# Optimization experiments

Hardware: AMD Instinct MI355X
Metric: run time of the kernel (lower is better)

Reference implementation:

```python
import jax, jax.numpy as jnp
import numpy as np
import math

B, S = 4, 1024
N_ITEMS, EMB = 50000, 128
H, D = 4, 32


def setup_inputs() -> dict:
    key = jax.random.key(0)
    ks = jax.random.split(key, 12)

    def lin(k, fan_in, fan_out):
        lim = 1.0 / math.sqrt(fan_in)
        return jax.random.uniform(k, (fan_in, fan_out), minval=-lim, maxval=lim, dtype=jnp.float32)

    inp = {}
    inp["sequence_item_indices"] = jax.random.randint(ks[0], (B, S), 0, N_ITEMS, dtype=jnp.int32)
    inp["sequence_correct_flags"] = jax.random.randint(ks[1], (B, S), 0, 2, dtype=jnp.int32)
    inp["sequence_time_gaps"] = jax.random.uniform(ks[2], (B, S), dtype=jnp.float32) * 100.0
    inp["item_emb"] = jax.random.normal(ks[3], (N_ITEMS, EMB), dtype=jnp.float32) * 0.02
    inp["ans_emb"] = jax.random.normal(ks[4], (2, EMB), dtype=jnp.float32) * 0.02
    inp["Wq"] = lin(ks[5], EMB, H * D); inp["bq"] = jnp.zeros((H * D,), jnp.float32)
    inp["Wk"] = lin(ks[6], EMB, H * D); inp["bk"] = jnp.zeros((H * D,), jnp.float32)
    inp["Wv"] = lin(ks[7], EMB, H * D); inp["bv"] = jnp.zeros((H * D,), jnp.float32)
    inp["Wh"] = lin(ks[8], 2 * EMB, EMB); inp["bh"] = jnp.zeros((EMB,), jnp.float32)
    inp["W1"] = lin(ks[9], H * D + EMB, EMB); inp["b1"] = jnp.zeros((EMB,), jnp.float32)
    inp["W2"] = lin(ks[10], EMB, 1); inp["b2"] = jnp.zeros((1,), jnp.float32)
    inp["theta_raw"] = jnp.zeros((H,), jnp.float32)
    return inp


def reference(sequence_item_indices, sequence_correct_flags, sequence_time_gaps,
              item_emb, ans_emb, Wq, bq, Wk, bk, Wv, bv, Wh, bh, W1, b1, W2, b2, theta_raw):
    Bb, Ss = sequence_item_indices.shape
    Hn = theta_raw.shape[0]
    Dd = Wq.shape[1] // Hn

    e = item_emb[sequence_item_indices]                      # [B,S,E]
    a = ans_emb[sequence_correct_flags]                      # [B,S,E]
    inter = jnp.concatenate([e, a], axis=-1) @ Wh + bh       # history_projection

    Q = (e @ Wq + bq).reshape(Bb, Ss, Hn, Dd)
    K = (e @ Wk + bk).reshape(Bb, Ss, Hn, Dd)
    V = (inter @ Wv + bv).reshape(Bb, Ss, Hn, Dd)
    scale = 1.0 / jnp.sqrt(jnp.float32(Dd))

    # self relevance per history position; per-target softmax over i<t done via exclusive prefix sums
    sr = jnp.sum(Q * K, axis=-1) * scale                     # [B,S,H]
    ex = jnp.exp(sr - jnp.max(sr, axis=1, keepdims=True))    # shift-invariant
    Ep = jnp.concatenate([jnp.zeros((Bb, 1, Hn), sr.dtype), jnp.cumsum(ex, axis=1)], axis=1)  # [B,S+1,H]

    g = jnp.maximum(sequence_time_gaps.astype(jnp.float32), 1.0)
    Pp = jnp.concatenate([jnp.zeros((Bb, 1), g.dtype), jnp.cumsum(g, axis=1)], axis=1)        # [B,S+1]

    t = jnp.arange(1, Ss)                                    # targets, T = S-1
    i = jnp.arange(Ss)                                       # history positions
    mask = i[None, :] < t[:, None]                           # [T,S]
    step = (t[:, None] - i[None, :]).astype(jnp.float32)     # arange(L,0,-1)[i] == t - i
    gap_diff = Pp[:, 1:Ss, None] - Pp[:, None, :Ss]          # [B,T,S]  sum_{j in [i,t)} clamp(gap,1)
    Et = Ep[:, 1:Ss, :]                                      # [B,T,H]  softmax normalizer Z_t
    rel = (Et[:, :, None, :] - Ep[:, None, :Ss, :]) / Et[:, :, None, :]  # cumulative relevance [B,T,S,H]
    pd = jnp.where(mask[None, :, :, None],
                   step[None, :, :, None] * gap_diff[..., None] * rel, 0.0)  # perceived distance

    theta = jax.nn.softplus(theta_raw) + 1e-4                # [H]
    decay = jnp.exp(-theta * pd)                             # [B,T,S,H]

    # candidate query at position t equals query_projection(item_embedding[t])
    raw = jnp.einsum('bthd,bihd->btih', Q[:, 1:], K) * scale # [B,T,S,H]
    scores = jnp.where(mask[None, :, :, None], raw * decay, -1e30)
    attn = jax.nn.softmax(scores, axis=2)                    # softmax over history positions
    ctx = jnp.einsum('btih,bihd->bthd', attn, V).reshape(Bb, Ss - 1, Hn * Dd)

    feat = jnp.concatenate([ctx, e[:, 1:]], axis=-1)
    h1 = jax.nn.relu(feat @ W1 + b1)                         # dropout is inference identity
    logit = (h1 @ W2 + b2)[..., 0]
    pred = jax.nn.sigmoid(logit)                             # [B,S-1]
    valid = jnp.ones((Bb, Ss - 1), dtype=bool)               # all positions valid (no padding)
    return pred, valid
```

## Files before the change

### kernel.cpp

```cpp
#include <hip/hip_runtime.h>
#include <math.h>

#define BSZ 4
#define SSZ 1024
#define EMBD 128
#define HN 4
#define DN 32
#define TQ (SSZ - 1)
#define NROWS (BSZ * TQ)

typedef __attribute__((ext_vector_type(8))) short bf16x8;
typedef __attribute__((ext_vector_type(4))) short bf16x4;
typedef __attribute__((ext_vector_type(4))) float f32x4;

static __device__ __forceinline__ unsigned short f2bf(float x) {
    union { float f; unsigned u; } v; v.f = x;
    unsigned r = v.u + 0x7fffu + ((v.u >> 16) & 1u);
    return (unsigned short)(r >> 16);
}
static __device__ __forceinline__ bf16x8 cvt8(const float4 a, const float4 b) {
    bf16x8 v;
    v[0] = (short)f2bf(a.x); v[1] = (short)f2bf(a.y);
    v[2] = (short)f2bf(a.z); v[3] = (short)f2bf(a.w);
    v[4] = (short)f2bf(b.x); v[5] = (short)f2bf(b.y);
    v[6] = (short)f2bf(b.z); v[7] = (short)f2bf(b.w);
    return v;
}

__global__ __launch_bounds__(256)
void embed4_kernel(const int* __restrict__ idx, const int* __restrict__ flg,
                   const float* __restrict__ item_emb, const float* __restrict__ ans_emb,
                   const float* __restrict__ Wq, const float* __restrict__ bq,
                   const float* __restrict__ Wk, const float* __restrict__ bk,
                   const float* __restrict__ Wv, const float* __restrict__ bv,
                   const float* __restrict__ Wh, const float* __restrict__ bh_bias,
                   unsigned short* __restrict__ Qts, unsigned short* __restrict__ Kts,
                   unsigned short* __restrict__ Vts,
                   float* __restrict__ ec, float* __restrict__ srw)
{
    __shared__ __align__(16) unsigned short esb[16][136];
    __shared__ __align__(16) unsigned short asb[16][136];
    __shared__ __align__(16) unsigned short intb[16][136];
    __shared__ __align__(16) unsigned short Wt[128][40];

    const int tid = threadIdx.x;
    const int tok0 = blockIdx.x * 16;
    const int b = blockIdx.x >> 6;
    const int s0 = tok0 & 1023;
    const int w = tid >> 6, lane = tid & 63;
    const int quad = lane >> 4, col = lane & 15;

    {
        const int tk = tid >> 4;
        const int d0 = (tid & 15) * 8;
        const int tok = tok0 + tk;
        const float* esrc = item_emb + (size_t)idx[tok] * EMBD + d0;
        const float* asrc = ans_emb + (size_t)flg[tok] * EMBD + d0;
        const float4 e0 = *(const float4*)esrc;
        const float4 e1 = *(const float4*)(esrc + 4);
        const float4 a0 = *(const float4*)asrc;
        const float4 a1 = *(const float4*)(asrc + 4);
        *(float4*)(ec + (size_t)tok * EMBD + d0) = e0;
        *(float4*)(ec + (size_t)tok * EMBD + d0 + 4) = e1;
        *(bf16x8*)&esb[tk][d0] = cvt8(e0, e1);
        *(bf16x8*)&asb[tk][d0] = cvt8(a0, a1);
    }

    const int jb = (tid & 31) * 4;
    const int ib = (tid >> 5) * 4;
    float rr[4][4];

    #define WSRC(R) ((R) < 8 ? Wh + (size_t)(R) * 4096                     \
                  : (R) < 12 ? Wq + (size_t)((R) - 8) * 4096               \
                  : (R) < 16 ? Wk + (size_t)((R) - 12) * 4096              \
                  : Wv + (size_t)((R) - 16) * 4096)
    #define LOADW(P)                                                       \
    {                                                                      \
        const float* _p = (P);                                             \
        *(float4*)rr[0] = *(const float4*)(_p + (ib + 0) * 128 + jb);      \
        *(float4*)rr[1] = *(const float4*)(_p + (ib + 1) * 128 + jb);      \
        *(float4*)rr[2] = *(const float4*)(_p + (ib + 2) * 128 + jb);      \
        *(float4*)rr[3] = *(const float4*)(_p + (ib + 3) * 128 + jb);      \
    }
    #define STOREW                                                         \
    {                                                                      \
        _Pragma("unroll")                                                  \
        for (int jj = 0; jj < 4; jj++) {                                   \
            bf16x4 v;                                                      \
            v[0] = (short)f2bf(rr[0][jj]); v[1] = (short)f2bf(rr[1][jj]);  \
            v[2] = (short)f2bf(rr[2][jj]); v[3] = (short)f2bf(rr[3][jj]);  \
            *(bf16x4*)&Wt[jb + jj][ib] = v;                                \
        }                                                                  \
    }

    f32x4 accI[2] = {{0.f,0.f,0.f,0.f},{0.f,0.f,0.f,0.f}};
    f32x4 accQ[2] = {{0.f,0.f,0.f,0.f},{0.f,0.f,0.f,0.f}};
    f32x4 accK[2] = {{0.f,0.f,0.f,0.f},{0.f,0.f,0.f,0.f}};
    f32x4 accV[2] = {{0.f,0.f,0.f,0.f},{0.f,0.f,0.f,0.f}};

    LOADW(WSRC(0));
    #pragma unroll
    for (int r = 0; r < 20; r++) {
        __syncthreads();
        STOREW;
        __syncthreads();
        if (r < 19) LOADW(WSRC(r + 1));

        const unsigned short (*Ab)[136] = (r < 4) ? esb : (r < 8) ? asb
                                        : (r < 16) ? esb : intb;
        const int koff = ((r < 8) ? (r & 3) : (r < 12) ? (r - 8)
                        : (r < 16) ? (r - 12) : (r - 16)) * 32;
        const bf16x8 af = *(const bf16x8*)&Ab[col][koff + quad * 8];
        f32x4* acc = (r < 8) ? accI : (r < 12) ? accQ : (r < 16) ? accK : accV;
        #pragma unroll
        for (int ntl = 0; ntl < 2; ntl++) {
            const bf16x8 bf = *(const bf16x8*)&Wt[w * 32 + ntl * 16 + col][quad * 8];
            acc[ntl] = __builtin_amdgcn_mfma_f32_16x16x32_bf16(af, bf, acc[ntl], 0, 0, 0);
        }
        if (r == 7) {
            #pragma unroll
            for (int ntl = 0; ntl < 2; ntl++) {
                const int j = w * 32 + ntl * 16 + col;
                const float bb = bh_bias[j];
                #pragma unroll
                for (int r4 = 0; r4 < 4; r4++)
                    intb[quad * 4 + r4][j] = f2bf(accI[ntl][r4] + bb);
            }
        }
    }
    #undef LOADW
    #undef STOREW
    #undef WSRC

    const int bhn = b * HN + w;
    const float scale = 0.17677669529663687f;
    float p[4] = {0.f, 0.f, 0.f, 0.f};
    #pragma unroll
    for (int ntl = 0; ntl < 2; ntl++) {
        const int j = w * 32 + ntl * 16 + col;
        const float bQ = bq[j], bK = bk[j], bV = bv[j];
        #pragma unroll
        for (int r = 0; r < 4; r++) {
            const float qv = accQ[ntl][r] + bQ;
            const float kv = accK[ntl][r] + bK;
            const int s = s0 + quad * 4 + r;
            const size_t o = ((size_t)bhn * SSZ + s) * DN + ntl * 16 + col;
            Qts[o] = f2bf(qv * scale);
            Kts[o] = f2bf(kv);
            Vts[o] = f2bf(accV[ntl][r] + bV);
            p[r] = fmaf(qv, kv, p[r]);
        }
    }
    #pragma unroll
    for (int r = 0; r < 4; r++) {
        float pr = p[r];
        pr += __shfl_xor(pr, 1, 64);
        pr += __shfl_xor(pr, 2, 64);
        pr += __shfl_xor(pr, 4, 64);
        pr += __shfl_xor(pr, 8, 64);
        if (col == 0)
            srw[(size_t)bhn * SSZ + s0 + quad * 4 + r] = pr * scale;
    }
}

__global__ __launch_bounds__(256)
void attn4_kernel(const unsigned short* __restrict__ Qts,
                  const unsigned short* __restrict__ Kts,
                  const unsigned short* __restrict__ Vts,
                  const float* __restrict__ srw, const float* __restrict__ gaps,
                  const float* __restrict__ theta_raw, float* __restrict__ csw)
{
    __shared__ __align__(16) unsigned short Ks[64][40];
    __shared__ __align__(16) unsigned short Vs[32][72];
    __shared__ __align__(16) unsigned short Ps[4][16][72];
    __shared__ float EpS[SSZ + 1];
    __shared__ float PpS[SSZ + 1];
    __shared__ float wtot[4];

    const int bid = blockIdx.x;
    const int qt = bid & 15;
    const int bh = bid >> 4;
    const int b = bh >> 2, h = bh & 3;
    const int tid = threadIdx.x;
    const int w = tid >> 6, lane = tid & 63;
    const int quad = lane >> 4, col = lane & 15;
    const int t0 = qt * 64 + 1;

    {
        const float4 sv = *(const float4*)(srw + (size_t)bh * SSZ + tid * 4);
        const float e0 = __expf(sv.x);
        const float p0 = e0;
        const float p1 = p0 + __expf(sv.y);
        const float p2 = p1 + __expf(sv.z);
        const float p3 = p2 + __expf(sv.w);
        float s = p3;
        #pragma unroll
        for (int d = 1; d < 64; d <<= 1) {
            const float t = __shfl_up(s, d, 64);
            if (lane >= d) s += t;
        }
        if (lane == 63) wtot[w] = s;
        __syncthreads();
        float base = s - p3;
        for (int ww = 0; ww < w; ww++) base += wtot[ww];
        EpS[tid * 4 + 1] = base + p0;
        EpS[tid * 4 + 2] = base + p1;
        EpS[tid * 4 + 3] = base + p2;
        EpS[tid * 4 + 4] = base + p3;
        if (tid == 0) EpS[0] = 0.0f;
    }
    {
        const float4 gv = *(const float4*)(gaps + (size_t)b * SSZ + tid * 4);
        const float p0 = fmaxf(gv.x, 1.0f);
        const float p1 = p0 + fmaxf(gv.y, 1.0f);
        const float p2 = p1 + fmaxf(gv.z, 1.0f);
        const float p3 = p2 + fmaxf(gv.w, 1.0f);
        float s = p3;
        #pragma unroll
        for (int d = 1; d < 64; d <<= 1) {
            const float t = __shfl_up(s, d, 64);
            if (lane >= d) s += t;
        }
        __syncthreads();
        if (lane == 63) wtot[w] = s;
        __syncthreads();
        float base = s - p3;
        for (int ww = 0; ww < w; ww++) base += wtot[ww];
        PpS[tid * 4 + 1] = base + p0;
        PpS[tid * 4 + 2] = base + p1;
        PpS[tid * 4 + 3] = base + p2;
        PpS[tid * 4 + 4] = base + p3;
        if (tid == 0) PpS[0] = 0.0f;
    }
    __syncthreads();

    const float theta = logf(1.0f + __expf(theta_raw[h])) + 1e-4f;
    const float nth = -theta;
    float Ept[4], Ppt[4], iEp[4], tft[4];
    int qrow[4], tq[4];
    #pragma unroll
    for (int r = 0; r < 4; r++) {
        qrow[r] = w * 16 + quad * 4 + r;
        tq[r] = t0 + qrow[r];
        tft[r] = (float)tq[r];
        Ept[r] = EpS[tq[r]];
        Ppt[r] = PpS[tq[r]];
        iEp[r] = 1.0f / Ept[r];
    }

    bf16x8 aq;
    {
        int t = t0 + w * 16 + col; if (t > 1023) t = 1023;
        aq = *(const bf16x8*)(Qts + ((size_t)(bh * SSZ + t)) * DN + quad * 8);
    }

    f32x4 acc0 = {0.f, 0.f, 0.f, 0.f};
    f32x4 acc1 = {0.f, 0.f, 0.f, 0.f};
    float lsum[4] = {0.f, 0.f, 0.f, 0.f};

    const int i_st = tid >> 2;
    const int d0 = (tid & 3) * 8;
    bf16x8 kreg = *(const bf16x8*)(Kts + ((size_t)(bh * SSZ + i_st)) * DN + d0);
    bf16x8 vreg = *(const bf16x8*)(Vts + ((size_t)(bh * SSZ + i_st)) * DN + d0);

    for (int c = 0; c <= qt; c++) {
        __syncthreads();
        *(bf16x8*)&Ks[i_st][d0] = kreg;
        #pragma unroll
        for (int k2 = 0; k2 < 8; k2++) Vs[d0 + k2][i_st] = (unsigned short)vreg[k2];
        __syncthreads();
        if (c < qt) {
            const size_t o = ((size_t)(bh * SSZ + (c + 1) * 64 + i_st)) * DN + d0;
            kreg = *(const bf16x8*)(Kts + o);
            vreg = *(const bf16x8*)(Vts + o);
        }

        const bool full = (c < qt);
        #pragma unroll
        for (int nt = 0; nt < 4; nt++) {
            const bf16x8 bk = *(const bf16x8*)&Ks[nt * 16 + col][quad * 8];
            f32x4 z = {0.f, 0.f, 0.f, 0.f};
            f32x4 raw = __builtin_amdgcn_mfma_f32_16x16x32_bf16(aq, bk, z, 0, 0, 0);
            const int il = nt * 16 + col;
            const int i_ = c * 64 + il;
            const float Epi = EpS[i_];
            const float Ppi = PpS[i_];
            const float fi = (float)i_;
            #pragma unroll
            for (int r = 0; r < 4; r++) {
                const float pdv = (tft[r] - fi) * (Ppt[r] - Ppi) * ((Ept[r] - Epi) * iEp[r]);
                const float sc  = raw[r] * __expf(nth * pdv);
                float p = __expf(sc);
                p = (full || il <= qrow[r]) ? p : 0.0f;
                lsum[r] += p;
                Ps[w][quad * 4 + r][il] = f2bf(p);
            }
        }
        #pragma unroll
        for (int ks = 0; ks < 2; ks++) {
            const bf16x8 ap = *(const bf16x8*)&Ps[w][col][ks * 32 + quad * 8];
            const bf16x8 bv0 = *(const bf16x8*)&Vs[col][ks * 32 + quad * 8];
            const bf16x8 bv1 = *(const bf16x8*)&Vs[16 + col][ks * 32 + quad * 8];
            acc0 = __builtin_amdgcn_mfma_f32_16x16x32_bf16(ap, bv0, acc0, 0, 0, 0);
            acc1 = __builtin_amdgcn_mfma_f32_16x16x32_bf16(ap, bv1, acc1, 0, 0, 0);
        }
    }

    #pragma unroll
    for (int r = 0; r < 4; r++) {
        float lr = lsum[r];
        #pragma unroll
        for (int msk = 8; msk >= 1; msk >>= 1) lr += __shfl_xor(lr, msk, 64);
        lsum[r] = 1.0f / lr;
    }
    #pragma unroll
    for (int r = 0; r < 4; r++) {
        if (tq[r] <= 1023) {
            float* dst = csw + ((size_t)(b * TQ + (tq[r] - 1))) * EMBD + h * DN;
            dst[col]      = acc0[r] * lsum[r];
            dst[16 + col] = acc1[r] * lsum[r];
        }
    }
}

__global__ __launch_bounds__(256)
void mlp3_kernel(const float* __restrict__ csw, const float* __restrict__ ec,
                 const float* __restrict__ W1, const float* __restrict__ b1,
                 const float* __restrict__ W2, const float* __restrict__ b2,
                 float* __restrict__ out)
{
    __shared__ __align__(16) unsigned short featb[32][264];
    __shared__ __align__(16) unsigned short W1t[128][264];
    __shared__ float sred[4][16];

    const int tid = threadIdx.x;
    const int r0 = blockIdx.x * 32;
    const int w = tid >> 6, lane = tid & 63;
    const int quad = lane >> 4, col = lane & 15;
    const int mt = w & 1, nh = w >> 1;

    {
        const int jb = (tid & 31) * 4;
        const int ib = (tid >> 5) * 4;
        for (int ic = 0; ic < 8; ic++) {
            const int i0 = ic * 32 + ib;
            float rr[4][4];
            *(float4*)rr[0] = *(const float4*)(W1 + (size_t)(i0 + 0) * 128 + jb);
            *(float4*)rr[1] = *(const float4*)(W1 + (size_t)(i0 + 1) * 128 + jb);
            *(float4*)rr[2] = *(const float4*)(W1 + (size_t)(i0 + 2) * 128 + jb);
            *(float4*)rr[3] = *(const float4*)(W1 + (size_t)(i0 + 3) * 128 + jb);
            #pragma unroll
            for (int jj = 0; jj < 4; jj++) {
                bf16x4 v;
                v[0] = (short)f2bf(rr[0][jj]); v[1] = (short)f2bf(rr[1][jj]);
                v[2] = (short)f2bf(rr[2][jj]); v[3] = (short)f2bf(rr[3][jj]);
                *(bf16x4*)&W1t[jb + jj][i0] = v;
            }
        }
    }
    {
        const int rr = tid >> 3;
        const int c0 = (tid & 7) * 32;
        int row = r0 + rr; if (row >= NROWS) row = NROWS - 1;
        const float* src;
        if (c0 < 128) {
            src = csw + (size_t)row * EMBD + c0;
        } else {
            const int bb = row / TQ;
            const int tt = row - bb * TQ + 1;
            src = ec + ((size_t)(bb * SSZ + tt)) * EMBD + (c0 - 128);
        }
        #pragma unroll
        for (int g = 0; g < 4; g++) {
            const float4 f0 = ((const float4*)src)[g * 2];
            const float4 f1 = ((const float4*)src)[g * 2 + 1];
            *(bf16x8*)&featb[rr][c0 + g * 8] = cvt8(f0, f1);
        }
    }
    __syncthreads();

    float s[4] = {0.f, 0.f, 0.f, 0.f};
    #pragma unroll
    for (int ntl = 0; ntl < 4; ntl++) {
        const int nt = nh * 4 + ntl;
        f32x4 acc = {0.f, 0.f, 0.f, 0.f};
        #pragma unroll
        for (int kc = 0; kc < 8; kc++) {
            const bf16x8 af = *(const bf16x8*)&featb[mt * 16 + col][kc * 32 + quad * 8];
            const bf16x8 bf = *(const bf16x8*)&W1t[nt * 16 + col][kc * 32 + quad * 8];
            acc = __builtin_amdgcn_mfma_f32_16x16x32_bf16(af, bf, acc, 0, 0, 0);
        }
        const int j = nt * 16 + col;
        const float b1j = b1[j], w2j = W2[j];
        #pragma unroll
        for (int r = 0; r < 4; r++)
            s[r] = fmaf(fmaxf(acc[r] + b1j, 0.0f), w2j, s[r]);
    }
    #pragma unroll
    for (int r = 0; r < 4; r++) {
        float sr = s[r];
        sr += __shfl_xor(sr, 1, 64);
        sr += __shfl_xor(sr, 2, 64);
        sr += __shfl_xor(sr, 4, 64);
        sr += __shfl_xor(sr, 8, 64);
        if (col == 0) sred[w][quad * 4 + r] = sr;
    }
    __syncthreads();
    if (tid < 32) {
        const int mt2 = tid >> 4, rr = tid & 15;
        const float logit = sred[mt2][rr] + sred[mt2 + 2][rr] + b2[0];
        const int grow = r0 + tid;
        if (grow < NROWS) {
            out[grow] = 1.0f / (1.0f + __expf(-logit));
            out[NROWS + grow] = 1.0f;
        }
    }
}

extern "C" void kernel_launch(void* const* d_in, const int* in_sizes, int n_in,
                              void* d_out, int out_size, void* d_ws, size_t ws_size,
                              hipStream_t stream)
{
    const int*   idx       = (const int*)d_in[0];
    const int*   flg       = (const int*)d_in[1];
    const float* gaps      = (const float*)d_in[2];
    const float* item_emb  = (const float*)d_in[3];
    const float* ans_emb   = (const float*)d_in[4];
    const float* Wq        = (const float*)d_in[5];
    const float* bq        = (const float*)d_in[6];
    const float* Wk        = (const float*)d_in[7];
    const float* bk        = (const float*)d_in[8];
    const float* Wv        = (const float*)d_in[9];
    const float* bv        = (const float*)d_in[10];
    const float* Wh        = (const float*)d_in[11];
    const float* bh        = (const float*)d_in[12];
    const float* W1        = (const float*)d_in[13];
    const float* b1        = (const float*)d_in[14];
    const float* W2        = (const float*)d_in[15];
    const float* b2        = (const float*)d_in[16];
    const float* theta_raw = (const float*)d_in[17];
    (void)in_sizes; (void)n_in; (void)ws_size;

    const size_t QKV = (size_t)BSZ * HN * SSZ * DN;
    unsigned short* Qts = (unsigned short*)d_ws;
    unsigned short* Kts = Qts + QKV;
    unsigned short* Vts = Kts + QKV;
    float* ec  = (float*)(Vts + QKV);
    float* srw = ec + (size_t)BSZ * SSZ * EMBD;
    float* csw = srw + (size_t)BSZ * HN * SSZ;

    float* out = (float*)d_out;

    embed4_kernel<<<BSZ * SSZ / 16, 256, 0, stream>>>(
        idx, flg, item_emb, ans_emb, Wq, bq, Wk, bk, Wv, bv, Wh, bh,
        Qts, Kts, Vts, ec, srw);
    attn4_kernel<<<BSZ * HN * 16, 256, 0, stream>>>(
        Qts, Kts, Vts, srw, gaps, theta_raw, csw);
    mlp3_kernel<<<(NROWS + 31) / 32, 256, 0, stream>>>(
        csw, ec, W1, b1, W2, b2, out);
}
```

Measured before the change: 149.4 us.

## Split attention history chunks across two blocks and merge partials in MLP

The attention kernel now launches twice as many blocks. Each query tile's causal history chunks are split into two halves, and each half writes an unnormalized context and a partial softmax denominator to separate buffers. The MLP kernel sums the two partial contexts and denominators, then normalizes before the bf16 conversion. This targets load imbalance and low occupancy from only 256 blocks with triangular work, at the cost of extra workspace traffic and a larger workspace footprint.

Result: faster. 145.3 us (median of 2 runs) (-2.8%).

```diff
diff --git a/kernel.cpp b/kernel.cpp
--- a/kernel.cpp
+++ b/kernel.cpp
@@ -168,7 +168,8 @@
                   const unsigned short* __restrict__ Kts,
                   const unsigned short* __restrict__ Vts,
                   const float* __restrict__ srw, const float* __restrict__ gaps,
-                  const float* __restrict__ theta_raw, float* __restrict__ csw)
+                  const float* __restrict__ theta_raw, float* __restrict__ csw,
+                  float* __restrict__ ls)
 {
     __shared__ __align__(16) unsigned short Ks[64][40];
     __shared__ __align__(16) unsigned short Vs[32][72];
@@ -178,13 +179,18 @@
     __shared__ float wtot[4];
 
     const int bid = blockIdx.x;
-    const int qt = bid & 15;
-    const int bh = bid >> 4;
+    const int half = bid & 1;
+    const int qt = (bid >> 1) & 15;
+    const int bh = bid >> 5;
     const int b = bh >> 2, h = bh & 3;
     const int tid = threadIdx.x;
     const int w = tid >> 6, lane = tid & 63;
     const int quad = lane >> 4, col = lane & 15;
     const int t0 = qt * 64 + 1;
+
+    const int nc = qt + 1;
+    const int c0r = half ? (nc >> 1) : 0;
+    const int c1r = half ? nc : (nc >> 1);
 
     {
         const float4 sv = *(const float4*)(srw + (size_t)bh * SSZ + tid * 4);
@@ -260,16 +266,16 @@
 
     const int i_st = tid >> 2;
     const int d0 = (tid & 3) * 8;
-    bf16x8 kreg = *(const bf16x8*)(Kts + ((size_t)(bh * SSZ + i_st)) * DN + d0);
-    bf16x8 vreg = *(const bf16x8*)(Vts + ((size_t)(bh * SSZ + i_st)) * DN + d0);
-
-    for (int c = 0; c <= qt; c++) {
+    bf16x8 kreg = *(const bf16x8*)(Kts + ((size_t)(bh * SSZ + c0r * 64 + i_st)) * DN + d0);
+    bf16x8 vreg = *(const bf16x8*)(Vts + ((size_t)(bh * SSZ + c0r * 64 + i_st)) * DN + d0);
+
+    for (int c = c0r; c < c1r; c++) {
         __syncthreads();
         *(bf16x8*)&Ks[i_st][d0] = kreg;
         #pragma unroll
         for (int k2 = 0; k2 < 8; k2++) Vs[d0 + k2][i_st] = (unsigned short)vreg[k2];
         __syncthreads();
-        if (c < qt) {
+        if (c + 1 < c1r) {
             const size_t o = ((size_t)(bh * SSZ + (c + 1) * 64 + i_st)) * DN + d0;
             kreg = *(const bf16x8*)(Kts + o);
             vreg = *(const bf16x8*)(Vts + o);
@@ -311,20 +317,24 @@
         float lr = lsum[r];
         #pragma unroll
         for (int msk = 8; msk >= 1; msk >>= 1) lr += __shfl_xor(lr, msk, 64);
-        lsum[r] = 1.0f / lr;
-    }
+        lsum[r] = lr;
+    }
+    const size_t cswh = (size_t)half * NROWS * EMBD;
+    const size_t lsh  = (size_t)half * (HN * BSZ * SSZ) + ((size_t)bh << 10);
     #pragma unroll
     for (int r = 0; r < 4; r++) {
         if (tq[r] <= 1023) {
-            float* dst = csw + ((size_t)(b * TQ + (tq[r] - 1))) * EMBD + h * DN;
-            dst[col]      = acc0[r] * lsum[r];
-            dst[16 + col] = acc1[r] * lsum[r];
+            float* dst = csw + cswh + ((size_t)(b * TQ + (tq[r] - 1))) * EMBD + h * DN;
+            dst[col]      = acc0[r];
+            dst[16 + col] = acc1[r];
+            if (col == 0) ls[lsh + tq[r]] = lsum[r];
         }
     }
 }
 
 __global__ __launch_bounds__(256)
-void mlp3_kernel(const float* __restrict__ csw, const float* __restrict__ ec,
+void mlp3_kernel(const float* __restrict__ csw, const float* __restrict__ ls,
+                 const float* __restrict__ ec,
                  const float* __restrict__ W1, const float* __restrict__ b1,
                  const float* __restrict__ W2, const float* __restrict__ b2,
                  float* __restrict__ out)
@@ -362,19 +372,38 @@
         const int rr = tid >> 3;
         const int c0 = (tid & 7) * 32;
         int row = r0 + rr; if (row >= NROWS) row = NROWS - 1;
-        const float* src;
         if (c0 < 128) {
-            src = csw + (size_t)row * EMBD + c0;
+            const int bb = row / TQ;
+            const int tt = row - bb * TQ + 1;
+            const int hh = c0 >> 5;
+            const size_t lsi = ((size_t)(bb * HN + hh) << 10) + tt;
+            const float l0 = ls[lsi];
+            const float l1 = ls[(size_t)(HN * BSZ * SSZ) + lsi];
+            const float inv = 1.0f / (l0 + l1);
+            const float* s0 = csw + (size_t)row * EMBD + c0;
+            const float* s1 = csw + (size_t)NROWS * EMBD + (size_t)row * EMBD + c0;
+            #pragma unroll
+            for (int g = 0; g < 4; g++) {
+                float4 f0 = ((const float4*)s0)[g * 2];
+                float4 f1 = ((const float4*)s0)[g * 2 + 1];
+                const float4 g0 = ((const float4*)s1)[g * 2];
+                const float4 g1 = ((const float4*)s1)[g * 2 + 1];
+                f0.x = (f0.x + g0.x) * inv; f0.y = (f0.y + g0.y) * inv;
+                f0.z = (f0.z + g0.z) * inv; f0.w = (f0.w + g0.w) * inv;
+                f1.x = (f1.x + g1.x) * inv; f1.y = (f1.y + g1.y) * inv;
+                f1.z = (f1.z + g1.z) * inv; f1.w = (f1.w + g1.w) * inv;
+                *(bf16x8*)&featb[rr][c0 + g * 8] = cvt8(f0, f1);
+            }
         } else {
             const int bb = row / TQ;
             const int tt = row - bb * TQ + 1;
-            src = ec + ((size_t)(bb * SSZ + tt)) * EMBD + (c0 - 128);
-        }
-        #pragma unroll
-        for (int g = 0; g < 4; g++) {
-            const float4 f0 = ((const float4*)src)[g * 2];
-            const float4 f1 = ((const float4*)src)[g * 2 + 1];
-            *(bf16x8*)&featb[rr][c0 + g * 8] = cvt8(f0, f1);
+            const float* src = ec + ((size_t)(bb * SSZ + tt)) * EMBD + (c0 - 128);
+            #pragma unroll
+            for (int g = 0; g < 4; g++) {
+                const float4 f0 = ((const float4*)src)[g * 2];
+                const float4 f1 = ((const float4*)src)[g * 2 + 1];
+                *(bf16x8*)&featb[rr][c0 + g * 8] = cvt8(f0, f1);
+            }
         }
     }
     __syncthreads();
@@ -448,14 +477,15 @@
     float* ec  = (float*)(Vts + QKV);
     float* srw = ec + (size_t)BSZ * SSZ * EMBD;
     float* csw = srw + (size_t)BSZ * HN * SSZ;
+    float* ls  = csw + 2 * (size_t)NROWS * EMBD;
 
     float* out = (float*)d_out;
 
     embed4_kernel<<<BSZ * SSZ / 16, 256, 0, stream>>>(
         idx, flg, item_emb, ans_emb, Wq, bq, Wk, bk, Wv, bv, Wh, bh,
         Qts, Kts, Vts, ec, srw);
-    attn4_kernel<<<BSZ * HN * 16, 256, 0, stream>>>(
-        Qts, Kts, Vts, srw, gaps, theta_raw, csw);
+    attn4_kernel<<<BSZ * HN * 32, 256, 0, stream>>>(
+        Qts, Kts, Vts, srw, gaps, theta_raw, csw, ls);
     mlp3_kernel<<<(NROWS + 31) / 32, 256, 0, stream>>>(
-        csw, ec, W1, b1, W2, b2, out);
-}
+        csw, ls, ec, W1, b1, W2, b2, out);
+}
```
